# Performance work log

Hardware: AMD Instinct MI355X
Metric: run time of the kernel (lower is better)

The kernel has to match this reference:

```python
import jax, jax.numpy as jnp
import numpy as np

B, S, D = 4, 2048, 512
H = 8
DH = D // H
NEG = -9e15


def setup_inputs() -> dict:
    key = jax.random.key(0)
    ks = jax.random.split(key, 6)
    x = jax.random.normal(ks[0], (B, S, D), dtype=jnp.float32)
    mask = jax.random.randint(ks[1], (B, S), 0, 2, dtype=jnp.int32)
    # Linear params (torch convention: W [out, in], y = x @ W.T + b)
    lim_qkv = 1.0 / np.sqrt(D)
    W_qkv = jax.random.uniform(ks[2], (3 * D, D), jnp.float32, -lim_qkv, lim_qkv)
    b_qkv = jax.random.uniform(ks[3], (3 * D,), jnp.float32, -lim_qkv, lim_qkv)
    lim_o = 1.0 / np.sqrt(D)
    W_o = jax.random.uniform(ks[4], (D, D), jnp.float32, -lim_o, lim_o)
    b_o = jax.random.uniform(ks[5], (D,), jnp.float32, -lim_o, lim_o)
    return {"x": x, "mask": mask, "W_qkv": W_qkv, "b_qkv": b_qkv, "W_o": W_o, "b_o": b_o}


def reference(x, mask, W_qkv, b_qkv, W_o, b_o):
    b, s, d = x.shape
    # fused QKV projection: [B,S,3D]
    qkv = jnp.einsum('bsd,ed->bse', x, W_qkv) + b_qkv
    qkv = qkv.reshape(b, s, H, 3 * DH).transpose(0, 2, 1, 3)  # [B,H,S,3*DH]
    q, k, v = jnp.split(qkv, 3, axis=-1)  # each [B,H,S,DH]
    logits = jnp.einsum('bhqd,bhkd->bhqk', q, k) / jnp.sqrt(jnp.float32(DH))
    m = mask[:, None, None, :]  # [B,1,1,S]
    logits = jnp.where(m == 0, jnp.float32(NEG), logits)
    attn = jax.nn.softmax(logits, axis=-1)  # [B,H,S,S]
    values = jnp.einsum('bhqk,bhkd->bhqd', attn, v)
    values = values.transpose(0, 2, 1, 3).reshape(b, s, d)
    o = jnp.einsum('bsd,ed->bse', values, W_o) + b_o
    return o
```

## Files before the change

kernel.cpp:

```cpp
#include <hip/hip_runtime.h>
#include <stdint.h>

#define Bv 4
#define Sv 2048
#define Dv 512
#define Hv 8
#define E3 1536

typedef unsigned short u16;
typedef __bf16 bf16x8 __attribute__((ext_vector_type(8)));
typedef float f32x4 __attribute__((ext_vector_type(4)));

__device__ __forceinline__ u16 f2b(float f) {
  union { float f; uint32_t u; } v; v.f = f;
  uint32_t r = v.u + 0x7FFFu + ((v.u >> 16) & 1u);
  return (u16)(r >> 16);
}

__device__ __forceinline__ void gl_lds16(const void* g, void* l) {
  __builtin_amdgcn_global_load_lds(
      (__attribute__((address_space(1))) void*)(uintptr_t)g,
      (__attribute__((address_space(3))) void*)(uintptr_t)l, 16, 0, 0);
}

__global__ __launch_bounds__(256) void k_cast(const float* __restrict__ in,
                                              u16* __restrict__ out, int n8) {
  int i = blockIdx.x * 256 + threadIdx.x;
  if (i >= n8) return;
  const float4* p = (const float4*)in;
  float4 a = p[(size_t)i * 2], b = p[(size_t)i * 2 + 1];
  union { u16 h[8]; uint4 v; } r;
  r.h[0] = f2b(a.x); r.h[1] = f2b(a.y); r.h[2] = f2b(a.z); r.h[3] = f2b(a.w);
  r.h[4] = f2b(b.x); r.h[5] = f2b(b.y); r.h[6] = f2b(b.z); r.h[7] = f2b(b.w);
  ((uint4*)out)[i] = r.v;
}

template <int OUTF32>
__global__ __launch_bounds__(256) void k_gemm_bt(const u16* __restrict__ A,
                                                 const u16* __restrict__ Bw,
                                                 const float* __restrict__ bias,
                                                 void* __restrict__ C, int N, int K) {
  __shared__ alignas(16) u16 As[128][32];
  __shared__ alignas(16) u16 Bs[128][32];
  const int tid = threadIdx.x, lane = tid & 63, w = tid >> 6;
  const int quad = lane >> 4, l16 = lane & 15;
  const int wm = w & 1, wn = w >> 1;
  const size_t m0 = (size_t)blockIdx.y * 128;
  const int n0 = blockIdx.x * 128;
  const int srow = lane >> 2, scol = (lane & 3) * 8;
  f32x4 acc[4][4] = {};
  for (int k0 = 0; k0 < K; k0 += 32) {
    #pragma unroll
    for (int c = 0; c < 2; ++c) {
      const int rb = (w * 2 + c) * 16;
      gl_lds16(A + (m0 + rb + srow) * K + k0 + scol, &As[rb][0]);
      gl_lds16(Bw + (size_t)(n0 + rb + srow) * K + k0 + scol, &Bs[rb][0]);
    }
    __syncthreads();
    bf16x8 af[4], bfr[4];
    #pragma unroll
    for (int t = 0; t < 4; ++t) {
      af[t]  = *(const bf16x8*)&As[wm * 64 + t * 16 + l16][quad * 8];
      bfr[t] = *(const bf16x8*)&Bs[wn * 64 + t * 16 + l16][quad * 8];
    }
    #pragma unroll
    for (int mt = 0; mt < 4; ++mt)
      #pragma unroll
      for (int nt = 0; nt < 4; ++nt)
        acc[mt][nt] = __builtin_amdgcn_mfma_f32_16x16x32_bf16(af[mt], bfr[nt],
                                                              acc[mt][nt], 0, 0, 0);
    __syncthreads();
  }
  #pragma unroll
  for (int nt = 0; nt < 4; ++nt) {
    const int col = n0 + wn * 64 + nt * 16 + l16;
    const float bv = bias[col];
    #pragma unroll
    for (int mt = 0; mt < 4; ++mt) {
      const size_t row = m0 + wm * 64 + mt * 16 + quad * 4;
      #pragma unroll
      for (int r = 0; r < 4; ++r) {
        float v = acc[mt][nt][r] + bv;
        if (OUTF32) ((float*)C)[(row + r) * N + col] = v;
        else        ((u16*)C)[(row + r) * N + col] = f2b(v);
      }
    }
  }
}

__global__ __launch_bounds__(256) void k_vtrans(const u16* __restrict__ qkv,
                                                const int* __restrict__ mask,
                                                u16* __restrict__ vt,
                                                float* __restrict__ mbias) {
  __shared__ alignas(16) u16 T[64][72];
  const int tid = threadIdx.x;
  const int bh = blockIdx.y, b = bh >> 3, h = bh & 7;
  const int s0 = blockIdx.x * 64;
  if (h == 0 && tid < 64) {
    const int s = b * Sv + s0 + tid;
    mbias[s] = mask[s] ? 0.0f : -1e30f;
  }
  for (int idx = tid; idx < 512; idx += 256) {
    int r = idx >> 3, c = idx & 7;
    *(uint4*)&T[r][c * 8] =
        *(const uint4*)(qkv + ((size_t)(b * Sv + s0 + r)) * E3 + h * 192 + 128 + c * 8);
  }
  __syncthreads();
  for (int idx = tid; idx < 512; idx += 256) {
    int d = idx >> 3, c = idx & 7;
    union { u16 h[8]; uint4 v; } rr;
    #pragma unroll
    for (int j = 0; j < 8; ++j) rr.h[j] = T[c * 8 + j][d];
    *(uint4*)(vt + ((size_t)(bh * 64 + d)) * Sv + s0 + c * 8) = rr.v;
  }
}

__global__ __launch_bounds__(256) void k_attn(const u16* __restrict__ qkv,
                                              const u16* __restrict__ vt,
                                              const float* __restrict__ mbias,
                                              u16* __restrict__ vals) {
  __shared__ alignas(16) u16 Ks[128][72];
  __shared__ alignas(16) u16 Vts[64][136];
  __shared__ alignas(16) u16 Ps[4][16][136];
  const int tid = threadIdx.x, lane = tid & 63, w = tid >> 6;
  const int quad = lane >> 4, l16 = lane & 15;
  const int bh = blockIdx.y, b = bh >> 3, h = bh & 7;
  const int q0 = blockIdx.x * 64 + w * 16;

  const u16* qrow = qkv + (size_t)(b * Sv + q0 + l16) * E3 + h * 192 + quad * 8;
  bf16x8 aq0 = *(const bf16x8*)qrow;
  bf16x8 aq1 = *(const bf16x8*)(qrow + 32);

  bf16x8 bones;
  {
    union { u16 u; __bf16 b; } one; one.u = 0x3F80;
    #pragma unroll
    for (int j = 0; j < 8; ++j) bones[j] = one.b;
  }

  f32x4 La = {0.f, 0.f, 0.f, 0.f};
  f32x4 Oa[4] = {};

  const u16* kgbase = qkv + (size_t)(b * Sv) * E3 + h * 192 + 64;
  const u16* vgbase = vt + (size_t)bh * 64 * Sv;
  const float* mrow = mbias + b * Sv + l16;
  u16* ps_w = &Ps[w][0][0];

  #pragma unroll 1
  for (int k0 = 0; k0 < Sv; k0 += 128) {
    for (int idx = tid; idx < 1024; idx += 256) {
      int r = idx >> 3, c = idx & 7;
      *(uint4*)&Ks[r][c * 8] = *(const uint4*)(kgbase + (size_t)(k0 + r) * E3 + c * 8);
    }
    for (int idx = tid; idx < 1024; idx += 256) {
      int d = idx >> 4, c = idx & 15;
      *(uint4*)&Vts[d][c * 8] = *(const uint4*)(vgbase + (size_t)d * Sv + k0 + c * 8);
    }
    __syncthreads();

    float mb[8];
    #pragma unroll
    for (int nt = 0; nt < 8; ++nt) mb[nt] = mrow[k0 + nt * 16];

    f32x4 Sa[8] = {};
    #pragma unroll
    for (int nt = 0; nt < 8; ++nt) {
      bf16x8 bk0 = *(const bf16x8*)&Ks[nt * 16 + l16][quad * 8];
      bf16x8 bk1 = *(const bf16x8*)&Ks[nt * 16 + l16][32 + quad * 8];
      Sa[nt] = __builtin_amdgcn_mfma_f32_16x16x32_bf16(aq0, bk0, Sa[nt], 0, 0, 0);
      Sa[nt] = __builtin_amdgcn_mfma_f32_16x16x32_bf16(aq1, bk1, Sa[nt], 0, 0, 0);
    }

    #pragma unroll
    for (int nt = 0; nt < 8; ++nt)
      #pragma unroll
      for (int r = 0; r < 4; ++r) {
        union { float f; uint32_t u; } pv;
        pv.f = __expf(fmaf(Sa[nt][r], 0.125f, mb[nt]));
        ps_w[(quad * 4 + r) * 136 + nt * 16 + l16] = (u16)(pv.u >> 16);
      }

    #pragma unroll
    for (int ks = 0; ks < 4; ++ks) {
      bf16x8 ap = *(const bf16x8*)(ps_w + l16 * 136 + ks * 32 + quad * 8);
      La = __builtin_amdgcn_mfma_f32_16x16x32_bf16(ap, bones, La, 0, 0, 0);
      #pragma unroll
      for (int nt2 = 0; nt2 < 4; ++nt2) {
        bf16x8 bv8 = *(const bf16x8*)&Vts[nt2 * 16 + l16][ks * 32 + quad * 8];
        Oa[nt2] = __builtin_amdgcn_mfma_f32_16x16x32_bf16(ap, bv8, Oa[nt2], 0, 0, 0);
      }
    }
    __syncthreads();
  }

  float li[4];
  #pragma unroll
  for (int r = 0; r < 4; ++r) li[r] = 1.0f / La[r];
  #pragma unroll
  for (int nt2 = 0; nt2 < 4; ++nt2)
    #pragma unroll
    for (int r = 0; r < 4; ++r) {
      const size_t srow = (size_t)(b * Sv + q0 + quad * 4 + r);
      vals[srow * Dv + h * 64 + nt2 * 16 + l16] = f2b(Oa[nt2][r] * li[r]);
    }
}

extern "C" void kernel_launch(void* const* d_in, const int* in_sizes, int n_in,
                              void* d_out, int out_size, void* d_ws, size_t ws_size,
                              hipStream_t stream) {
  const float* x    = (const float*)d_in[0];
  const int*   mask = (const int*)d_in[1];
  const float* Wqkv = (const float*)d_in[2];
  const float* bqkv = (const float*)d_in[3];
  const float* Wo   = (const float*)d_in[4];
  const float* bo   = (const float*)d_in[5];
  float* out = (float*)d_out;

  char* ws = (char*)d_ws;
  u16* xb    = (u16*)(ws + 0);
  u16* wqkvb = (u16*)(ws + 8388608);
  u16* wob   = (u16*)(ws + 9961472);
  u16* qkv   = (u16*)(ws + 10485760);
  u16* vt    = (u16*)(ws + 35651584);
  u16* vals  = (u16*)(ws + 44040192);
  float* mbias = (float*)(ws + 0);

  k_cast<<<2048, 256, 0, stream>>>(x, xb, 524288);
  k_cast<<<384, 256, 0, stream>>>(Wqkv, wqkvb, 98304);
  k_cast<<<128, 256, 0, stream>>>(Wo, wob, 32768);
  k_gemm_bt<0><<<dim3(12, 64), 256, 0, stream>>>(xb, wqkvb, bqkv, qkv, E3, Dv);
  k_vtrans<<<dim3(32, 32), 256, 0, stream>>>(qkv, mask, vt, mbias);
  k_attn<<<dim3(32, 32), 256, 0, stream>>>(qkv, vt, mbias, vals);
  k_gemm_bt<1><<<dim3(4, 64), 256, 0, stream>>>(vals, wob, bo, out, Dv, Dv);
}
```

Baseline: 250.3 us.

## Prepack K/V in MFMA fragment order and read directly from global in attention

```diff
diff --git a/kernel.cpp b/kernel.cpp
--- a/kernel.cpp
+++ b/kernel.cpp
@@ -88,10 +88,11 @@
   }
 }
 
-__global__ __launch_bounds__(256) void k_vtrans(const u16* __restrict__ qkv,
-                                                const int* __restrict__ mask,
-                                                u16* __restrict__ vt,
-                                                float* __restrict__ mbias) {
+__global__ __launch_bounds__(256) void k_pack(const u16* __restrict__ qkv,
+                                              const int* __restrict__ mask,
+                                              u16* __restrict__ kp,
+                                              u16* __restrict__ vp,
+                                              float* __restrict__ mbias) {
   __shared__ alignas(16) u16 T[64][72];
   const int tid = threadIdx.x;
   const int bh = blockIdx.y, b = bh >> 3, h = bh & 7;
@@ -100,27 +101,35 @@
     const int s = b * Sv + s0 + tid;
     mbias[s] = mask[s] ? 0.0f : -1e30f;
   }
+  const size_t kpb = (size_t)bh * 128 * 1024;
+  for (int idx = tid; idx < 512; idx += 256) {
+    int r = idx >> 3, c8 = idx & 7;
+    uint4 d = *(const uint4*)(qkv + (size_t)(b * Sv + s0 + r) * E3 + h * 192 + 64 + c8 * 8);
+    int tile = (s0 >> 4) + (r >> 4), half = c8 >> 2, quad = c8 & 3, l16 = r & 15;
+    *(uint4*)(kp + kpb + (size_t)tile * 1024 + half * 512 + (quad * 16 + l16) * 8) = d;
+  }
   for (int idx = tid; idx < 512; idx += 256) {
     int r = idx >> 3, c = idx & 7;
     *(uint4*)&T[r][c * 8] =
         *(const uint4*)(qkv + ((size_t)(b * Sv + s0 + r)) * E3 + h * 192 + 128 + c * 8);
   }
   __syncthreads();
+  const size_t vpb = (size_t)bh * 64 * 2048;
   for (int idx = tid; idx < 512; idx += 256) {
-    int d = idx >> 3, c = idx & 7;
+    int cc = idx >> 8, rest = idx & 255, dh = rest >> 2, kq = rest & 3;
     union { u16 h[8]; uint4 v; } rr;
     #pragma unroll
-    for (int j = 0; j < 8; ++j) rr.h[j] = T[c * 8 + j][d];
-    *(uint4*)(vt + ((size_t)(bh * 64 + d)) * Sv + s0 + c * 8) = rr.v;
+    for (int j = 0; j < 8; ++j) rr.h[j] = T[cc * 32 + kq * 8 + j][dh];
+    int chunk = (s0 >> 5) + cc, nt2 = dh >> 4;
+    *(uint4*)(vp + vpb + ((size_t)(chunk * 4 + nt2)) * 512 + (kq * 16 + (dh & 15)) * 8) = rr.v;
   }
 }
 
 __global__ __launch_bounds__(256) void k_attn(const u16* __restrict__ qkv,
-                                              const u16* __restrict__ vt,
+                                              const u16* __restrict__ kp,
+                                              const u16* __restrict__ vp,
                                               const float* __restrict__ mbias,
                                               u16* __restrict__ vals) {
-  __shared__ alignas(16) u16 Ks[128][72];
-  __shared__ alignas(16) u16 Vts[64][136];
   __shared__ alignas(16) u16 Ps[4][16][136];
   const int tid = threadIdx.x, lane = tid & 63, w = tid >> 6;
   const int quad = lane >> 4, l16 = lane & 15;
@@ -141,56 +150,44 @@
   f32x4 La = {0.f, 0.f, 0.f, 0.f};
   f32x4 Oa[4] = {};
 
-  const u16* kgbase = qkv + (size_t)(b * Sv) * E3 + h * 192 + 64;
-  const u16* vgbase = vt + (size_t)bh * 64 * Sv;
+  const u16* kpb = kp + (size_t)bh * 128 * 1024 + lane * 8;
+  const u16* vpb = vp + (size_t)bh * 64 * 2048 + lane * 8;
   const float* mrow = mbias + b * Sv + l16;
   u16* ps_w = &Ps[w][0][0];
+  const float cs = 0.18033688011112042f;
 
   #pragma unroll 1
   for (int k0 = 0; k0 < Sv; k0 += 128) {
-    for (int idx = tid; idx < 1024; idx += 256) {
-      int r = idx >> 3, c = idx & 7;
-      *(uint4*)&Ks[r][c * 8] = *(const uint4*)(kgbase + (size_t)(k0 + r) * E3 + c * 8);
-    }
-    for (int idx = tid; idx < 1024; idx += 256) {
-      int d = idx >> 4, c = idx & 15;
-      *(uint4*)&Vts[d][c * 8] = *(const uint4*)(vgbase + (size_t)d * Sv + k0 + c * 8);
-    }
-    __syncthreads();
-
-    float mb[8];
-    #pragma unroll
-    for (int nt = 0; nt < 8; ++nt) mb[nt] = mrow[k0 + nt * 16];
-
+    const int t0 = k0 >> 4, c0 = k0 >> 5;
     f32x4 Sa[8] = {};
     #pragma unroll
     for (int nt = 0; nt < 8; ++nt) {
-      bf16x8 bk0 = *(const bf16x8*)&Ks[nt * 16 + l16][quad * 8];
-      bf16x8 bk1 = *(const bf16x8*)&Ks[nt * 16 + l16][32 + quad * 8];
+      const u16* tb = kpb + (size_t)(t0 + nt) * 1024;
+      bf16x8 bk0 = *(const bf16x8*)tb;
+      bf16x8 bk1 = *(const bf16x8*)(tb + 512);
       Sa[nt] = __builtin_amdgcn_mfma_f32_16x16x32_bf16(aq0, bk0, Sa[nt], 0, 0, 0);
       Sa[nt] = __builtin_amdgcn_mfma_f32_16x16x32_bf16(aq1, bk1, Sa[nt], 0, 0, 0);
     }
-
-    #pragma unroll
-    for (int nt = 0; nt < 8; ++nt)
+    #pragma unroll
+    for (int nt = 0; nt < 8; ++nt) {
+      const float mb = mrow[k0 + nt * 16];
       #pragma unroll
       for (int r = 0; r < 4; ++r) {
         union { float f; uint32_t u; } pv;
-        pv.f = __expf(fmaf(Sa[nt][r], 0.125f, mb[nt]));
+        pv.f = __builtin_amdgcn_exp2f(fmaf(Sa[nt][r], cs, mb));
         ps_w[(quad * 4 + r) * 136 + nt * 16 + l16] = (u16)(pv.u >> 16);
       }
-
+    }
     #pragma unroll
     for (int ks = 0; ks < 4; ++ks) {
       bf16x8 ap = *(const bf16x8*)(ps_w + l16 * 136 + ks * 32 + quad * 8);
       La = __builtin_amdgcn_mfma_f32_16x16x32_bf16(ap, bones, La, 0, 0, 0);
       #pragma unroll
       for (int nt2 = 0; nt2 < 4; ++nt2) {
-        bf16x8 bv8 = *(const bf16x8*)&Vts[nt2 * 16 + l16][ks * 32 + quad * 8];
+        bf16x8 bv8 = *(const bf16x8*)(vpb + (size_t)((c0 + ks) * 4 + nt2) * 512);
         Oa[nt2] = __builtin_amdgcn_mfma_f32_16x16x32_bf16(ap, bv8, Oa[nt2], 0, 0, 0);
       }
     }
-    __syncthreads();
   }
 
   float li[4];
@@ -221,15 +218,16 @@
   u16* wqkvb = (u16*)(ws + 8388608);
   u16* wob   = (u16*)(ws + 9961472);
   u16* qkv   = (u16*)(ws + 10485760);
-  u16* vt    = (u16*)(ws + 35651584);
+  u16* kp    = (u16*)(ws + 35651584);
   u16* vals  = (u16*)(ws + 44040192);
-  float* mbias = (float*)(ws + 0);
+  u16* vp    = (u16*)(ws + 0);
+  float* mbias = (float*)(ws + 8388608);
 
   k_cast<<<2048, 256, 0, stream>>>(x, xb, 524288);
   k_cast<<<384, 256, 0, stream>>>(Wqkv, wqkvb, 98304);
   k_cast<<<128, 256, 0, stream>>>(Wo, wob, 32768);
   k_gemm_bt<0><<<dim3(12, 64), 256, 0, stream>>>(xb, wqkvb, bqkv, qkv, E3, Dv);
-  k_vtrans<<<dim3(32, 32), 256, 0, stream>>>(qkv, mask, vt, mbias);
-  k_attn<<<dim3(32, 32), 256, 0, stream>>>(qkv, vt, mbias, vals);
+  k_pack<<<dim3(32, 32), 256, 0, stream>>>(qkv, mask, kp, vp, mbias);
+  k_attn<<<dim3(32, 32), 256, 0, stream>>>(qkv, kp, vp, mbias, vals);
   k_gemm_bt<1><<<dim3(4, 64), 256, 0, stream>>>(vals, wob, bo, out, Dv, Dv);
 }
```

Measured after the change: 218.1 us. -12.9%, faster.
